# Performance work log

Hardware: AMD Instinct MI355X
Metric: run time of the kernel (lower is better)

The kernel has to match this reference:

```python
import jax, jax.numpy as jnp
import numpy as np

NUM_HEADS = 12
HEAD_DIM = 64


def _rotate_half(x):
    x1, x2 = jnp.split(x, 2, axis=-1)
    return jnp.concatenate([-x2, x1], axis=-1)


def setup_inputs() -> dict:
    key = jax.random.key(0)
    ks = jax.random.split(key, 5)
    B, S, H = 4, 2048, 768
    x = jax.random.normal(ks[0], (B, S, H), dtype=jnp.float32)
    # rope tables per (batch, position, head_dim)
    pos = jnp.arange(S, dtype=jnp.float32)[:, None]
    inv = 1.0 / (10000.0 ** (jnp.arange(0, HEAD_DIM, 2, dtype=jnp.float32) / HEAD_DIM))
    ang = pos * inv[None, :]  # [S, hd/2]
    ang = jnp.concatenate([ang, ang], axis=-1)  # [S, hd]
    cos = jnp.broadcast_to(jnp.cos(ang)[None], (B, S, HEAD_DIM)).astype(jnp.float32)
    sin = jnp.broadcast_to(jnp.sin(ang)[None], (B, S, HEAD_DIM)).astype(jnp.float32)
    Wqkv = jax.random.normal(ks[1], (3 * H, H), dtype=jnp.float32) * 0.02
    Wo = jax.random.normal(ks[2], (H, H), dtype=jnp.float32) * 0.02
    return {"x": x, "cos": cos, "sin": sin, "Wqkv": Wqkv, "Wo": Wo, "window": 64}


def reference(x, cos, sin, Wqkv, Wo, window):
    B, S, H = x.shape
    nh, hd = NUM_HEADS, HEAD_DIM
    scale = hd ** -0.5
    qkv = jnp.einsum('bsh,oh->bso', x, Wqkv)  # [B,S,3H]
    qkv = qkv.reshape(B, S, 3, nh, hd)
    q = qkv[:, :, 0].transpose(0, 2, 1, 3)  # [B,nh,S,hd]
    k = qkv[:, :, 1].transpose(0, 2, 1, 3)
    v = qkv[:, :, 2].transpose(0, 2, 1, 3)
    # RoPE in float32, cos/sin broadcast over heads: [B,1,S,hd]
    c = cos[:, None].astype(jnp.float32)
    s = sin[:, None].astype(jnp.float32)
    qf, kf = q.astype(jnp.float32), k.astype(jnp.float32)
    q = (qf * c + _rotate_half(qf) * s).astype(q.dtype)
    k = (kf * c + _rotate_half(kf) * s).astype(k.dtype)
    scores = jnp.einsum('bhqd,bhkd->bhqk', q, k) * scale
    idx = jnp.arange(S)
    band = jnp.abs(idx[:, None] - idx[None, :]) <= window  # sliding-window mask
    scores = jnp.where(band[None, None], scores, -jnp.inf)
    probs = jax.nn.softmax(scores, axis=-1)
    y = jnp.einsum('bhqk,bhkd->bhqd', probs, v)  # [B,nh,S,hd]
    y = y.transpose(0, 2, 1, 3).reshape(B, S, H)
    return jnp.einsum('bsh,oh->bso', y, Wo)
```

## Files before the change

### kernel.cpp

```cpp
#include <hip/hip_runtime.h>


typedef __attribute__((ext_vector_type(8))) _Float16 f16x8;
typedef __attribute__((ext_vector_type(4))) float    f32x4;

#define BDIM 4
#define SDIM 2048
#define HDIM 768
#define NH   12
#define HD   64
#define NQKV 2304
#define MROWS 8192

__device__ __forceinline__ void gload16(const void* g, void* l) {
    __builtin_amdgcn_global_load_lds(
        (__attribute__((address_space(1))) void*)(g),
        (__attribute__((address_space(3))) void*)(l),
        16, 0, 0);
}

__global__ __launch_bounds__(256) void cvt_f32_f16(
    const float* __restrict__ src, _Float16* __restrict__ dst, int n8)
{
    int i = blockIdx.x * 256 + threadIdx.x;
    if (i >= n8) return;
    const float4* s4 = (const float4*)src + (long)i * 2;
    float4 a = s4[0], b = s4[1];
    f16x8 o;
    o[0] = (_Float16)a.x; o[1] = (_Float16)a.y;
    o[2] = (_Float16)a.z; o[3] = (_Float16)a.w;
    o[4] = (_Float16)b.x; o[5] = (_Float16)b.y;
    o[6] = (_Float16)b.z; o[7] = (_Float16)b.w;
    *((f16x8*)dst + i) = o;
}

template <int EPI>
__global__ __launch_bounds__(256) void gemm_kernel(
    const _Float16* __restrict__ A,
    const _Float16* __restrict__ Bt,
    float* __restrict__ C,
    const float* __restrict__ cosp,
    const float* __restrict__ sinp,
    _Float16* __restrict__ qh,
    _Float16* __restrict__ kh,
    _Float16* __restrict__ vh,
    int M, int N, int K)
{
    __shared__ __align__(16) _Float16 lsA[128 * 32];
    __shared__ __align__(16) _Float16 lsB[128 * 32];

    int nTn = N >> 7;
    int nwg = gridDim.x;
    int bid = blockIdx.x;
    int wg = bid;
    if ((nwg & 7) == 0) {
        int cpx = nwg >> 3;
        wg = (bid & 7) * cpx + (bid >> 3);
    }
    int tm = wg / nTn, tn = wg % nTn;
    int m0 = tm << 7, n0 = tn << 7;

    int tid  = threadIdx.x;
    int lane = tid & 63;
    int w    = tid >> 6;
    int wr   = w >> 1, wc = w & 1;
    int l15  = lane & 15, lk = lane >> 4;

    f32x4 acc[4][4] = {};

    int srow = tid >> 2;
    int scol = (tid & 3) << 3;
    const _Float16* ga0 = A  + (long)(m0 + srow) * K + scol;
    const _Float16* gb0 = Bt + (long)(n0 + srow) * K + scol;
    _Float16* la = &lsA[tid * 8];
    _Float16* lb = &lsB[tid * 8];
    const long gstep = (long)64 * K;

    for (int k0 = 0; k0 < K; k0 += 32) {
        __syncthreads();
        gload16(ga0 + k0,         la);
        gload16(ga0 + gstep + k0, la + 2048);
        gload16(gb0 + k0,         lb);
        gload16(gb0 + gstep + k0, lb + 2048);
        __syncthreads();

        f16x8 af[4], bfr[4];
#pragma unroll
        for (int m = 0; m < 4; ++m)
            af[m] = *(const f16x8*)&lsA[(wr * 64 + m * 16 + l15) * 32 + lk * 8];
#pragma unroll
        for (int n = 0; n < 4; ++n)
            bfr[n] = *(const f16x8*)&lsB[(wc * 64 + n * 16 + l15) * 32 + lk * 8];
#pragma unroll
        for (int m = 0; m < 4; ++m)
#pragma unroll
            for (int n = 0; n < 4; ++n)
                acc[m][n] = __builtin_amdgcn_mfma_f32_16x16x32_f16(
                    af[m], bfr[n], acc[m][n], 0, 0, 0);
    }

    if (EPI == 0) {
#pragma unroll
        for (int m = 0; m < 4; ++m)
#pragma unroll
            for (int n = 0; n < 4; ++n)
#pragma unroll
                for (int j = 0; j < 4; ++j) {
                    int gr = m0 + wr * 64 + m * 16 + lk * 4 + j;
                    int gc = n0 + wc * 64 + n * 16 + l15;
                    C[(long)gr * N + gc] = acc[m][n][j];
                }
    } else {
        int ht = (n0 >> 6) + wc;
        int t  = ht / NH;
        int h  = ht - t * NH;
        int b  = m0 >> 11;
        long base_bh = ((long)(b * NH + h)) * SDIM;
#pragma unroll
        for (int m = 0; m < 4; ++m) {
#pragma unroll
            for (int j = 0; j < 4; ++j) {
                int gr = m0 + wr * 64 + m * 16 + lk * 4 + j;
                int s  = gr & (SDIM - 1);
                if (t == 2) {
#pragma unroll
                    for (int n = 0; n < 4; ++n) {
                        int d = n * 16 + l15;
                        vh[(base_bh + s) * HD + d] = (_Float16)acc[m][n][j];
                    }
                } else {
                    float vals[4];
#pragma unroll
                    for (int n = 0; n < 4; ++n) vals[n] = acc[m][n][j];
#pragma unroll
                    for (int n = 0; n < 4; ++n) {
                        int d = n * 16 + l15;
                        float cc = cosp[(long)gr * HD + d];
                        float ss = sinp[(long)gr * HD + d];
                        float pv = (n < 2) ? -vals[n + 2] : vals[n - 2];
                        float o  = vals[n] * cc + pv * ss;
                        long oidx = (base_bh + s) * HD + d;
                        if (t == 0) qh[oidx] = (_Float16)o;
                        else        kh[oidx] = (_Float16)o;
                    }
                }
            }
        }
    }
}

#define SSTR 200
#define PSTR 200
__global__ __launch_bounds__(256) void attn_mfma(
    const _Float16* __restrict__ qh,
    const _Float16* __restrict__ kh,
    const _Float16* __restrict__ vh,
    _Float16* __restrict__ yh)
{
    __shared__ __align__(16) _Float16 lsVT[64 * SSTR];
    __shared__ __align__(16) _Float16 lsP [64 * PSTR];

    int bid = blockIdx.x;
    int qt  = bid & 31;
    int bh  = bid >> 5;
    int q0  = qt << 6;
    int k0  = q0 - 64;
    int tid = threadIdx.x;
    int lane = tid & 63;
    int w = tid >> 6;
    int l15 = lane & 15, lg = lane >> 4;

    const _Float16* Qb = qh + (long)bh * SDIM * HD;
    const _Float16* Kb = kh + (long)bh * SDIM * HD;
    const _Float16* Vb = vh + (long)bh * SDIM * HD;

#pragma unroll
    for (int c = 0; c < 3; ++c) {
        int rk = c * 64 + lane;
        int s  = k0 + rk;
        s = s < 0 ? 0 : (s >= SDIM ? SDIM - 1 : s);
        const f16x8* vr = (const f16x8*)(Vb + (long)s * HD + w * 16);
        f16x8 v0 = vr[0], v1 = vr[1];
#pragma unroll
        for (int e = 0; e < 8; ++e) {
            lsVT[(w * 16 + e)     * SSTR + rk] = v0[e];
            lsVT[(w * 16 + 8 + e) * SSTR + rk] = v1[e];
        }
    }

    int qrow = q0 + w * 16 + l15;
    const f16x8* qp = (const f16x8*)(Qb + (long)qrow * HD + lg * 8);
    f16x8 qa0 = qp[0];
    f16x8 qa1 = qp[4];

    float sums[4] = {0.f, 0.f, 0.f, 0.f};
    int iqb = w * 16 + lg * 4;
#pragma unroll 4
    for (int kt = 0; kt < 12; ++kt) {
        int krow = k0 + kt * 16 + l15;
        int kcl = krow < 0 ? 0 : (krow >= SDIM ? SDIM - 1 : krow);
        const f16x8* kp = (const f16x8*)(Kb + (long)kcl * HD + lg * 8);
        f16x8 kb0 = kp[0], kb1 = kp[4];
        f32x4 acc = {0.f, 0.f, 0.f, 0.f};
        acc = __builtin_amdgcn_mfma_f32_16x16x32_f16(qa0, kb0, acc, 0, 0, 0);
        acc = __builtin_amdgcn_mfma_f32_16x16x32_f16(qa1, kb1, acc, 0, 0, 0);
        int jk = kt * 16 + l15;
        bool kin = (krow >= 0) && (krow < SDIM);
#pragma unroll
        for (int j = 0; j < 4; ++j) {
            int i = iqb + j;
            bool valid = kin && (jk >= i) && (jk <= i + 128);
            float p = valid ? __expf(acc[j] * 0.125f) : 0.f;
            sums[j] += p;
            lsP[(w * 16 + lg * 4 + j) * PSTR + jk] = (_Float16)p;
        }
    }

#pragma unroll
    for (int m = 1; m < 16; m <<= 1) {
#pragma unroll
        for (int j = 0; j < 4; ++j)
            sums[j] += __shfl_xor(sums[j], m, 64);
    }
    float inv[4];
#pragma unroll
    for (int j = 0; j < 4; ++j) inv[j] = 1.f / sums[j];

    __syncthreads();

    f32x4 accy[4] = {};
    const _Float16* prow = &lsP[(w * 16 + l15) * PSTR + lg * 8];
#pragma unroll
    for (int kc = 0; kc < 6; ++kc) {
        f16x8 pa = *(const f16x8*)(prow + kc * 32);
#pragma unroll
        for (int dt = 0; dt < 4; ++dt) {
            f16x8 vb = *(const f16x8*)&lsVT[(dt * 16 + l15) * SSTR + kc * 32 + lg * 8];
            accy[dt] = __builtin_amdgcn_mfma_f32_16x16x32_f16(pa, vb, accy[dt], 0, 0, 0);
        }
    }

    int b = bh / NH, h = bh - (bh / NH) * NH;
    long outbase = ((long)b * SDIM) * HDIM + (long)h * HD;
#pragma unroll
    for (int dt = 0; dt < 4; ++dt) {
#pragma unroll
        for (int j = 0; j < 4; ++j) {
            int srow = q0 + w * 16 + lg * 4 + j;
            yh[outbase + (long)srow * HDIM + dt * 16 + l15] =
                (_Float16)(accy[dt][j] * inv[j]);
        }
    }
}

extern "C" void kernel_launch(void* const* d_in, const int* in_sizes, int n_in,
                              void* d_out, int out_size, void* d_ws, size_t ws_size,
                              hipStream_t stream)
{
    const float* x    = (const float*)d_in[0];
    const float* cosp = (const float*)d_in[1];
    const float* sinp = (const float*)d_in[2];
    const float* Wqkv = (const float*)d_in[3];
    const float* Wo   = (const float*)d_in[4];
    float* out = (float*)d_out;

    char* ws = (char*)d_ws;
    _Float16* xh    = (_Float16*)(ws);
    _Float16* wqkvh = (_Float16*)(ws + 12582912);
    _Float16* woh   = (_Float16*)(ws + 16121856);
    _Float16* qh    = (_Float16*)(ws + 17301504);
    _Float16* kh    = (_Float16*)(ws + 29884416);
    _Float16* vh    = (_Float16*)(ws + 42467328);
    _Float16* yh    = (_Float16*)(ws + 55050240);

    cvt_f32_f16<<<(MROWS * HDIM / 8 + 255) / 256, 256, 0, stream>>>(x, xh, MROWS * HDIM / 8);
    cvt_f32_f16<<<(NQKV * HDIM / 8 + 255) / 256, 256, 0, stream>>>(Wqkv, wqkvh, NQKV * HDIM / 8);
    cvt_f32_f16<<<(HDIM * HDIM / 8 + 255) / 256, 256, 0, stream>>>(Wo, woh, HDIM * HDIM / 8);

    {
        dim3 grid((MROWS / 128) * (NQKV / 128));
        gemm_kernel<1><<<grid, 256, 0, stream>>>(
            xh, wqkvh, nullptr, cosp, sinp, qh, kh, vh, MROWS, NQKV, HDIM);
    }

    {
        dim3 grid(BDIM * NH * (SDIM / 64));
        attn_mfma<<<grid, 256, 0, stream>>>(qh, kh, vh, yh);
    }

    {
        dim3 grid((MROWS / 128) * (HDIM / 128));
        gemm_kernel<0><<<grid, 256, 0, stream>>>(
            yh, woh, out, nullptr, nullptr, nullptr, nullptr, nullptr,
            MROWS, HDIM, HDIM);
    }
}
```

Measured before the change: 122.0 us.

## Load GEMM fragments directly from global memory with register double buffering

Replaces the LDS-staged GEMM main loop, which used global_load_lds and two barriers per k-step, with direct per-lane global loads of MFMA fragments into registers. Two fragment sets are ping-ponged so the next k-slice loads while the current one feeds the MFMAs. This removes the LDS round trip and the block-wide syncs. In exchange, operands shared by the four waves are fetched separately by each wave, relying on L1/L2 for reuse, and register pressure rises. The XCD workgroup remap is also made unconditional.

```diff
diff --git a/kernel.cpp b/kernel.cpp
--- a/kernel.cpp
+++ b/kernel.cpp
@@ -11,13 +11,6 @@
 #define HD   64
 #define NQKV 2304
 #define MROWS 8192
-
-__device__ __forceinline__ void gload16(const void* g, void* l) {
-    __builtin_amdgcn_global_load_lds(
-        (__attribute__((address_space(1))) void*)(g),
-        (__attribute__((address_space(3))) void*)(l),
-        16, 0, 0);
-}
 
 __global__ __launch_bounds__(256) void cvt_f32_f16(
     const float* __restrict__ src, _Float16* __restrict__ dst, int n8)
@@ -35,7 +28,7 @@
 }
 
 template <int EPI>
-__global__ __launch_bounds__(256) void gemm_kernel(
+__global__ __launch_bounds__(256) void gemm_direct(
     const _Float16* __restrict__ A,
     const _Float16* __restrict__ Bt,
     float* __restrict__ C,
@@ -46,17 +39,11 @@
     _Float16* __restrict__ vh,
     int M, int N, int K)
 {
-    __shared__ __align__(16) _Float16 lsA[128 * 32];
-    __shared__ __align__(16) _Float16 lsB[128 * 32];
-
     int nTn = N >> 7;
     int nwg = gridDim.x;
     int bid = blockIdx.x;
-    int wg = bid;
-    if ((nwg & 7) == 0) {
-        int cpx = nwg >> 3;
-        wg = (bid & 7) * cpx + (bid >> 3);
-    }
+    int cpx = nwg >> 3;
+    int wg  = (bid & 7) * cpx + (bid >> 3);
     int tm = wg / nTn, tn = wg % nTn;
     int m0 = tm << 7, n0 = tn << 7;
 
@@ -66,82 +53,85 @@
     int wr   = w >> 1, wc = w & 1;
     int l15  = lane & 15, lk = lane >> 4;
 
+    const _Float16* pa[4];
+    const _Float16* pb[4];
+#pragma unroll
+    for (int mf = 0; mf < 4; ++mf)
+        pa[mf] = A + (long)(m0 + wr * 64 + mf * 16 + l15) * K + lk * 8;
+#pragma unroll
+    for (int nf = 0; nf < 4; ++nf)
+        pb[nf] = Bt + (long)(n0 + wc * 64 + nf * 16 + l15) * K + lk * 8;
+
     f32x4 acc[4][4] = {};
-
-    int srow = tid >> 2;
-    int scol = (tid & 3) << 3;
-    const _Float16* ga0 = A  + (long)(m0 + srow) * K + scol;
-    const _Float16* gb0 = Bt + (long)(n0 + srow) * K + scol;
-    _Float16* la = &lsA[tid * 8];
-    _Float16* lb = &lsB[tid * 8];
-    const long gstep = (long)64 * K;
-
-    for (int k0 = 0; k0 < K; k0 += 32) {
-        __syncthreads();
-        gload16(ga0 + k0,         la);
-        gload16(ga0 + gstep + k0, la + 2048);
-        gload16(gb0 + k0,         lb);
-        gload16(gb0 + gstep + k0, lb + 2048);
-        __syncthreads();
-
-        f16x8 af[4], bfr[4];
-#pragma unroll
-        for (int m = 0; m < 4; ++m)
-            af[m] = *(const f16x8*)&lsA[(wr * 64 + m * 16 + l15) * 32 + lk * 8];
-#pragma unroll
-        for (int n = 0; n < 4; ++n)
-            bfr[n] = *(const f16x8*)&lsB[(wc * 64 + n * 16 + l15) * 32 + lk * 8];
-#pragma unroll
-        for (int m = 0; m < 4; ++m)
-#pragma unroll
-            for (int n = 0; n < 4; ++n)
-                acc[m][n] = __builtin_amdgcn_mfma_f32_16x16x32_f16(
-                    af[m], bfr[n], acc[m][n], 0, 0, 0);
-    }
-
-    if (EPI == 0) {
-#pragma unroll
-        for (int m = 0; m < 4; ++m)
-#pragma unroll
-            for (int n = 0; n < 4; ++n)
+    f16x8 a0[4], b0[4], a1[4], b1[4];
+
+#define LD(av, bv, kk) do {                                              \
+        _Pragma("unroll")                                                \
+        for (int i = 0; i < 4; ++i) av[i] = *(const f16x8*)(pa[i] + (kk)); \
+        _Pragma("unroll")                                                \
+        for (int i = 0; i < 4; ++i) bv[i] = *(const f16x8*)(pb[i] + (kk)); \
+    } while (0)
+#define MM(av, bv)                                                       \
+    _Pragma("unroll")                                                    \
+    for (int mf = 0; mf < 4; ++mf)                                       \
+        _Pragma("unroll")                                                \
+        for (int nf = 0; nf < 4; ++nf)                                   \
+            acc[mf][nf] = __builtin_amdgcn_mfma_f32_16x16x32_f16(        \
+                av[mf], bv[nf], acc[mf][nf], 0, 0, 0);
+
+    LD(a0, b0, 0);
+    for (int k = 0; k < K; k += 64) {
+        LD(a1, b1, k + 32);
+        MM(a0, b0);
+        if (k + 64 < K) LD(a0, b0, k + 64);
+        MM(a1, b1);
+    }
+#undef LD
+#undef MM
+
+    if constexpr (EPI == 0) {
+#pragma unroll
+        for (int mf = 0; mf < 4; ++mf)
+#pragma unroll
+            for (int nf = 0; nf < 4; ++nf)
 #pragma unroll
                 for (int j = 0; j < 4; ++j) {
-                    int gr = m0 + wr * 64 + m * 16 + lk * 4 + j;
-                    int gc = n0 + wc * 64 + n * 16 + l15;
-                    C[(long)gr * N + gc] = acc[m][n][j];
+                    int gr = m0 + wr * 64 + mf * 16 + lk * 4 + j;
+                    int gc = n0 + wc * 64 + nf * 16 + l15;
+                    C[(long)gr * N + gc] = acc[mf][nf][j];
                 }
     } else {
         int ht = (n0 >> 6) + wc;
-        int t  = ht / NH;
-        int h  = ht - t * NH;
+        int tq = ht / NH;
+        int h  = ht - tq * NH;
         int b  = m0 >> 11;
         long base_bh = ((long)(b * NH + h)) * SDIM;
 #pragma unroll
-        for (int m = 0; m < 4; ++m) {
+        for (int mf = 0; mf < 4; ++mf) {
 #pragma unroll
             for (int j = 0; j < 4; ++j) {
-                int gr = m0 + wr * 64 + m * 16 + lk * 4 + j;
+                int gr = m0 + wr * 64 + mf * 16 + lk * 4 + j;
                 int s  = gr & (SDIM - 1);
-                if (t == 2) {
-#pragma unroll
-                    for (int n = 0; n < 4; ++n) {
-                        int d = n * 16 + l15;
-                        vh[(base_bh + s) * HD + d] = (_Float16)acc[m][n][j];
+                if (tq == 2) {
+#pragma unroll
+                    for (int nf = 0; nf < 4; ++nf) {
+                        int d = nf * 16 + l15;
+                        vh[(base_bh + s) * HD + d] = (_Float16)acc[mf][nf][j];
                     }
                 } else {
                     float vals[4];
 #pragma unroll
-                    for (int n = 0; n < 4; ++n) vals[n] = acc[m][n][j];
-#pragma unroll
-                    for (int n = 0; n < 4; ++n) {
-                        int d = n * 16 + l15;
+                    for (int nf = 0; nf < 4; ++nf) vals[nf] = acc[mf][nf][j];
+#pragma unroll
+                    for (int nf = 0; nf < 4; ++nf) {
+                        int d = nf * 16 + l15;
                         float cc = cosp[(long)gr * HD + d];
                         float ss = sinp[(long)gr * HD + d];
-                        float pv = (n < 2) ? -vals[n + 2] : vals[n - 2];
-                        float o  = vals[n] * cc + pv * ss;
+                        float pv = (nf < 2) ? -vals[nf + 2] : vals[nf - 2];
+                        float o  = vals[nf] * cc + pv * ss;
                         long oidx = (base_bh + s) * HD + d;
-                        if (t == 0) qh[oidx] = (_Float16)o;
-                        else        kh[oidx] = (_Float16)o;
+                        if (tq == 0) qh[oidx] = (_Float16)o;
+                        else         kh[oidx] = (_Float16)o;
                     }
                 }
             }
@@ -279,7 +269,7 @@
 
     {
         dim3 grid((MROWS / 128) * (NQKV / 128));
-        gemm_kernel<1><<<grid, 256, 0, stream>>>(
+        gemm_direct<1><<<grid, 256, 0, stream>>>(
             xh, wqkvh, nullptr, cosp, sinp, qh, kh, vh, MROWS, NQKV, HDIM);
     }
 
@@ -290,7 +280,7 @@
 
     {
         dim3 grid((MROWS / 128) * (HDIM / 128));
-        gemm_kernel<0><<<grid, 256, 0, stream>>>(
+        gemm_direct<0><<<grid, 256, 0, stream>>>(
             yh, woh, out, nullptr, nullptr, nullptr, nullptr, nullptr,
             MROWS, HDIM, HDIM);
     }
```

New measurement: 221.1 us. 81.2% more time.
